# Performance work log

Hardware: AMD Instinct MI355X
Metric: run time of the kernel (lower is better)

The kernel has to match this reference:

```python
import jax, jax.numpy as jnp
import numpy as np
import math

D_MODEL = 512; NHEAD = 8; D_FF = 2048
DS_HEADS = 4; DS_DEPTH = 156; EPS = 1e-5
B = 128; N = 300; M = 300


def _ln(x, g, b):
    m = x.mean(-1, keepdims=True)
    v = ((x - m) ** 2).mean(-1, keepdims=True)
    return (x - m) / jnp.sqrt(v + EPS) * g + b


def _mish(x):
    return x * jnp.tanh(jax.nn.softplus(x))


def _mha(xq, xk, xv, in_w, in_b, out_w, out_b, nhead):
    D = xq.shape[-1]; dh = D // nhead
    wq, wk, wv = jnp.split(in_w, 3, axis=0)
    bq, bk, bv = jnp.split(in_b, 3)
    def proj(x, w, b):
        y = x @ w.T + b
        Bm, Nn, _ = y.shape
        return y.reshape(Bm, Nn, nhead, dh).transpose(0, 2, 1, 3)
    q, k, v = proj(xq, wq, bq), proj(xk, wk, bk), proj(xv, wv, bv)
    s = jnp.einsum('bhqd,bhkd->bhqk', q, k) / math.sqrt(dh)
    p = jax.nn.softmax(s, axis=-1)
    o = jnp.einsum('bhqk,bhkd->bhqd', p, v)
    Bm, _, Nn, _ = o.shape
    o = o.transpose(0, 2, 1, 3).reshape(Bm, Nn, D)
    return o @ out_w.T + out_b


def _custom_weight(p):
    # sequential kinematic-tree averaging on the post-softmax [...,24,24] matrix
    def upd(p, i, j, si, sj):
        return p.at[..., i, j].set((p[..., i, j] + p[..., si, sj]) * 0.5)
    p = upd(p, 0, 6, 0, 3); p = upd(p, 6, 0, 3, 0)
    p = upd(p, 0, 9, 0, 6); p = upd(p, 9, 0, 6, 0)
    for idx in (12, 13, 14):
        p = upd(p, 0, idx, 0, 9); p = upd(p, idx, 0, 9, 0)
    for s, tgt in ((13, 16), (14, 17), (12, 15)):
        p = upd(p, 0, tgt, 0, s); p = upd(p, tgt, 0, s, 0)
    return p


def _ds_attn(x, qk_w, v_w, lw, lb):
    Bm, Nn, _ = x.shape
    comb = jnp.einsum('bnf,fx->bnx', x, qk_w)
    q, k = jnp.split(comb, 2, axis=2)
    v = jnp.einsum('bnf,fx->bnx', x, v_w)
    def heads(y):
        return y.reshape(Bm, Nn, DS_HEADS, DS_DEPTH).transpose(0, 2, 1, 3)
    q, k, v = heads(q), heads(k), heads(v)  # [B,H,N,156]
    qs = q[..., 3:147].reshape(Bm, DS_HEADS, Nn, 24, 6)
    ks = k[..., 3:147].reshape(Bm, DS_HEADS, Nn, 24, 6)
    vs = v[..., 3:147].reshape(Bm, DS_HEADS, Nn, 24, 6)
    s = jnp.einsum('bhnij,bhnkj->bhnik', qs, ks) / math.sqrt(6.0)
    p = _custom_weight(jax.nn.softmax(s, axis=-1))
    o = jnp.einsum('bhnik,bhnkj->bhnij', p, vs).reshape(Bm, DS_HEADS, Nn, 144)
    v = v.at[..., 3:147].set(o)
    v = v.transpose(0, 2, 1, 3).reshape(Bm, Nn, DS_HEADS * DS_DEPTH)
    return v @ lw.T + lb


def _align(x_d, t, w, b):
    tt = t + x_d.mean(axis=-2)           # [B,D]
    h = _mish(tt) @ w.T + b              # [B,2D]
    weight, bias = jnp.split(h, 2, axis=-1)
    return (weight[:, None, :] + 1.0) * x_d + bias[:, None, :]


def _forward(tgt, memory, t, qk_w, v_w, ds_lw, ds_lb,
             ta_in_w, ta_in_b, ta_out_w, ta_out_b,
             ca_in_w, ca_in_b, ca_out_w, ca_out_b,
             l1_w, l1_b, l2_w, l2_b,
             n1_g, n1_b, n2_g, n2_b, n3_g, n3_b, n4_g, n4_b,
             a1_w, a1_b, a2_w, a2_b, a3_w, a3_b):
    x = tgt
    x = x + _ds_attn(_ln(x, n1_g, n1_b), qk_w, v_w, ds_lw, ds_lb)
    xn = _ln(x, n2_g, n2_b)
    x2 = _mha(xn, xn, xn, ta_in_w, ta_in_b, ta_out_w, ta_out_b, NHEAD)
    x = x + _align(x2, t, a1_w, a1_b)
    x3 = _mha(_ln(x, n3_g, n3_b), memory, memory, ca_in_w, ca_in_b, ca_out_w, ca_out_b, NHEAD)
    x = x + _align(x3, t, a2_w, a2_b)
    xn4 = _ln(x, n4_g, n4_b)
    x4 = jax.nn.relu(xn4 @ l1_w.T + l1_b) @ l2_w.T + l2_b
    x = x + _align(x4, t, a3_w, a3_b)
    return x


def setup_inputs():
    key = jax.random.key(0)
    ks = iter(jax.random.split(key, 64))
    def nrm(shape, s=0.02):
        return jax.random.normal(next(ks), shape, dtype=jnp.float32) * s
    z = lambda *shape: jnp.zeros(shape, jnp.float32)
    o = lambda *shape: jnp.ones(shape, jnp.float32)
    D = D_MODEL
    inp = {
        'tgt': jax.random.normal(next(ks), (B, N, D), dtype=jnp.float32),
        'memory': jax.random.normal(next(ks), (B, M, D), dtype=jnp.float32),
        't': jax.random.normal(next(ks), (B, D), dtype=jnp.float32),
        'qk_w': nrm((D, 2 * DS_DEPTH * DS_HEADS)),
        'v_w': nrm((D, DS_DEPTH * DS_HEADS)),
        'ds_lw': nrm((D, DS_DEPTH * DS_HEADS)), 'ds_lb': z(D),
        'ta_in_w': nrm((3 * D, D)), 'ta_in_b': z(3 * D),
        'ta_out_w': nrm((D, D)), 'ta_out_b': z(D),
        'ca_in_w': nrm((3 * D, D)), 'ca_in_b': z(3 * D),
        'ca_out_w': nrm((D, D)), 'ca_out_b': z(D),
        'l1_w': nrm((D_FF, D)), 'l1_b': z(D_FF),
        'l2_w': nrm((D, D_FF)), 'l2_b': z(D),
        'n1_g': o(D), 'n1_b': z(D), 'n2_g': o(D), 'n2_b': z(D),
        'n3_g': o(D), 'n3_b': z(D), 'n4_g': o(D), 'n4_b': z(D),
        'a1_w': nrm((2 * D, D)), 'a1_b': z(2 * D),
        'a2_w': nrm((2 * D, D)), 'a2_b': z(2 * D),
        'a3_w': nrm((2 * D, D)), 'a3_b': z(2 * D),
        'cond_drop_prob': 0,
    }
    return inp


def reference(tgt, memory, t, qk_w, v_w, ds_lw, ds_lb,
              ta_in_w, ta_in_b, ta_out_w, ta_out_b,
              ca_in_w, ca_in_b, ca_out_w, ca_out_b,
              l1_w, l1_b, l2_w, l2_b,
              n1_g, n1_b, n2_g, n2_b, n3_g, n3_b, n4_g, n4_b,
              a1_w, a1_b, a2_w, a2_b, a3_w, a3_b, cond_drop_prob):
    # cond_drop_prob is unused in the torch forward body (dropout eval mode)
    return _forward(tgt, memory, t, qk_w, v_w, ds_lw, ds_lb,
                    ta_in_w, ta_in_b, ta_out_w, ta_out_b,
                    ca_in_w, ca_in_b, ca_out_w, ca_out_b,
                    l1_w, l1_b, l2_w, l2_b,
                    n1_g, n1_b, n2_g, n2_b, n3_g, n3_b, n4_g, n4_b,
                    a1_w, a1_b, a2_w, a2_b, a3_w, a3_b)
```

## Files before the change

kernel.cpp:

```cpp
#include <hip/hip_runtime.h>
#include <math.h>

#define DEV __device__ __forceinline__

static constexpr int BB   = 128;
static constexpr int NN   = 300;
static constexpr int DM   = 512;

typedef __attribute__((ext_vector_type(8))) short short8;
typedef __attribute__((ext_vector_type(4))) float f32x4;

DEV unsigned short f2bf(float f) {
  unsigned u = __float_as_uint(f);
  unsigned r = (u + 0x7fffu + ((u >> 16) & 1u)) >> 16;
  return (unsigned short)r;
}
DEV float bf2f(unsigned short s) { return __uint_as_float((unsigned)s << 16); }
DEV unsigned pack_bf16x2(float a, float b) {
  return (unsigned)f2bf(a) | ((unsigned)f2bf(b) << 16);
}
DEV unsigned pack_trunc(float a, float b) {
  return (__float_as_uint(a) >> 16) | (__float_as_uint(b) & 0xffff0000u);
}

DEV void gld16(const void* g, void* l) {
  __builtin_amdgcn_global_load_lds(
      (const __attribute__((address_space(1))) unsigned int*)g,
      (__attribute__((address_space(3))) unsigned int*)l,
      16, 0, 0);
}

__global__ __launch_bounds__(256) void ln_kernel(
    const float* __restrict__ X, const float* __restrict__ g,
    const float* __restrict__ b, unsigned short* __restrict__ Y, int rows)
{
  int wv = threadIdx.x >> 6, lane = threadIdx.x & 63;
  int row = blockIdx.x * 4 + wv;
  if (row >= rows) return;
  const float* xp = X + (size_t)row * DM;
  float v[8]; float s = 0.f, s2 = 0.f;
#pragma unroll
  for (int j = 0; j < 8; j++) {
    v[j] = xp[lane + 64 * j]; s += v[j]; s2 += v[j] * v[j];
  }
#pragma unroll
  for (int o = 32; o >= 1; o >>= 1) { s += __shfl_xor(s, o); s2 += __shfl_xor(s2, o); }
  float mean = s * (1.f / 512.f);
  float var  = s2 * (1.f / 512.f) - mean * mean;
  float rstd = rsqrtf(var + 1e-5f);
  unsigned short* yp = Y + (size_t)row * DM;
#pragma unroll
  for (int j = 0; j < 8; j++) {
    int c = lane + 64 * j;
    yp[c] = f2bf((v[j] - mean) * rstd * g[c] + b[c]);
  }
}

__global__ __launch_bounds__(256) void cvt_bf16(
    const float* __restrict__ in, unsigned short* __restrict__ out, int n4)
{
  int i = blockIdx.x * 256 + threadIdx.x;
  if (i >= n4) return;
  float4 v = ((const float4*)in)[i];
  union { unsigned short s[4]; uint2 u; } o;
  o.s[0] = f2bf(v.x); o.s[1] = f2bf(v.y); o.s[2] = f2bf(v.z); o.s[3] = f2bf(v.w);
  *(uint2*)&out[(size_t)i * 4] = o.u;
}

__global__ __launch_bounds__(256) void cvt_pad_bf16(
    const float* __restrict__ in, unsigned short* __restrict__ out,
    int R, int C, int Cpad)
{
  int idx = blockIdx.x * 256 + threadIdx.x;
  int r = idx / Cpad, c = idx % Cpad;
  if (r >= R) return;
  out[idx] = (c < C) ? f2bf(in[(size_t)r * C + c]) : (unsigned short)0;
}

__global__ __launch_bounds__(256) void transpose_bf16(
    const float* __restrict__ in, unsigned short* __restrict__ out,
    int R, int Ccols, int Cpad)
{
  __shared__ float t[32][33];
  int c0 = blockIdx.x * 32, r0 = blockIdx.y * 32;
  int x = threadIdx.x & 31, y = threadIdx.x >> 5;
#pragma unroll
  for (int dy = 0; dy < 32; dy += 8) {
    int r = r0 + y + dy, c = c0 + x;
    t[y + dy][x] = (r < R && c < Ccols) ? in[(size_t)r * Ccols + c] : 0.f;
  }
  __syncthreads();
#pragma unroll
  for (int dy = 0; dy < 32; dy += 8) {
    int c = c0 + y + dy, r = r0 + x;
    if (c < Cpad && r < R) out[(size_t)c * R + r] = f2bf(t[x][y + dy]);
  }
}

template<int EPI>
__global__ __launch_bounds__(256) void gemm_bb(
    const unsigned short* __restrict__ A, int lda,
    const unsigned short* __restrict__ W, int ldw,
    const float* __restrict__ bias,
    const float* __restrict__ R, int ldr,
    void* __restrict__ Cv, int ldc,
    int M, int K, int NC)
{
  __shared__ __align__(16) unsigned short As[128 * 32];
  __shared__ __align__(16) unsigned short Bs[128 * 32];
  const int tid = threadIdx.x;
  const int wave = tid >> 6, lane = tid & 63;
  const int wr = wave >> 1, wc = wave & 1;
  const int quad = lane >> 4, l16 = lane & 15;

  const unsigned nx = gridDim.x, nwg = nx * gridDim.y;
  const unsigned orig = blockIdx.y * nx + blockIdx.x;
  const unsigned qq = nwg >> 3, rr = nwg & 7;
  const unsigned xcd = orig & 7, idx = orig >> 3;
  const unsigned swz = (xcd < rr) ? (xcd * (qq + 1) + idx)
                                  : (rr * (qq + 1) + (xcd - rr) * qq + idx);
  const int n0 = (int)(swz % nx) * 128;
  const int m0 = (int)(swz / nx) * 128;

  int ra = m0 + (tid >> 2);
  int ra0 = (ra      >= M) ? M - 1 : ra;
  int ra1 = (ra + 64 >= M) ? M - 1 : ra + 64;
  const unsigned short* a0 = A + (size_t)ra0 * lda + (tid & 3) * 8;
  const unsigned short* a1 = A + (size_t)ra1 * lda + (tid & 3) * 8;
  const unsigned short* b0 = W + (size_t)(n0 + (tid >> 2)) * ldw + (tid & 3) * 8;
  const unsigned short* b1 = b0 + (size_t)64 * ldw;
  unsigned short* dA0 = &As[wave * 512];
  unsigned short* dA1 = &As[2048 + wave * 512];
  unsigned short* dB0 = &Bs[wave * 512];
  unsigned short* dB1 = &Bs[2048 + wave * 512];

  f32x4 acc[4][4];
#pragma unroll
  for (int i = 0; i < 4; i++)
#pragma unroll
    for (int j = 0; j < 4; j++) acc[i][j] = (f32x4){0.f, 0.f, 0.f, 0.f};

  for (int k0 = 0; k0 < K; k0 += 32) {
    gld16(a0 + k0, dA0);
    gld16(a1 + k0, dA1);
    gld16(b0 + k0, dB0);
    gld16(b1 + k0, dB1);
    __syncthreads();
    short8 af[4], bq[4];
#pragma unroll
    for (int i = 0; i < 4; i++)
      af[i] = *(const short8*)&As[(wr * 64 + i * 16 + l16) * 32 + quad * 8];
#pragma unroll
    for (int j = 0; j < 4; j++)
      bq[j] = *(const short8*)&Bs[(wc * 64 + j * 16 + l16) * 32 + quad * 8];
#pragma unroll
    for (int i = 0; i < 4; i++)
#pragma unroll
      for (int j = 0; j < 4; j++)
        acc[i][j] = __builtin_amdgcn_mfma_f32_16x16x32_bf16(af[i], bq[j], acc[i][j], 0, 0, 0);
    __syncthreads();
  }

#pragma unroll
  for (int i = 0; i < 4; i++) {
    int rbase = m0 + wr * 64 + i * 16 + quad * 4;
#pragma unroll
    for (int r = 0; r < 4; r++) {
      int row = rbase + r;
      if (row < M) {
        size_t rowc = (size_t)row * ldc;
#pragma unroll
        for (int j = 0; j < 4; j++) {
          int col = n0 + wc * 64 + j * 16 + l16;
          if (col < NC) {
            float e = acc[i][j][r];
            if (EPI == 1 || EPI == 2 || EPI == 3 || EPI == 5) e += bias[col];
            if (EPI == 3) e += R[(size_t)row * ldr + col];
            if (EPI == 2) {
              ((unsigned short*)Cv)[rowc + col] = f2bf(fmaxf(e, 0.f));
            } else if (EPI == 5 || EPI == 6) {
              ((unsigned short*)Cv)[rowc + col] = f2bf(e);
            } else {
              ((float*)Cv)[rowc + col] = e;
            }
          }
        }
      }
    }
  }
}

__global__ __launch_bounds__(256) void ds_attn_kernel(
    const float* __restrict__ COMB, unsigned short* __restrict__ V)
{
  __shared__ float ks[4][2][24][6];
  __shared__ float vs[4][2][24][6];
  int wv = threadIdx.x >> 6, lane = threadIdx.x & 63;
  int half = lane >> 5, i = lane & 31;
  int u  = blockIdx.x * 4 + wv;
  int bn = u >> 1, hp = u & 1;
  int h  = hp * 2 + half;
  size_t cbase = (size_t)bn * 1248 + h * 156 + 3;
  size_t vbase = (size_t)bn * 640  + h * 156 + 3;

  float q[6];
  if (i < 24) {
#pragma unroll
    for (int j = 0; j < 6; j++) {
      q[j]                 = COMB[cbase + i * 6 + j];
      ks[wv][half][i][j]   = COMB[cbase + 624 + i * 6 + j];
      vs[wv][half][i][j]   = bf2f(V[vbase + i * 6 + j]);
    }
  } else {
#pragma unroll
    for (int j = 0; j < 6; j++) q[j] = 0.f;
  }
  __syncthreads();

  float p[24];
#pragma unroll
  for (int k = 0; k < 24; k++) p[k] = 0.f;

  if (i < 24) {
    float mx = -1e30f;
#pragma unroll
    for (int k = 0; k < 24; k++) {
      float s = 0.f;
#pragma unroll
      for (int j = 0; j < 6; j++) s += q[j] * ks[wv][half][k][j];
      s *= 0.4082482904638631f;
      p[k] = s; mx = fmaxf(mx, s);
    }
    float sum = 0.f;
#pragma unroll
    for (int k = 0; k < 24; k++) { p[k] = __expf(p[k] - mx); sum += p[k]; }
    float inv = 1.f / sum;
#pragma unroll
    for (int k = 0; k < 24; k++) p[k] *= inv;
  }

  {
    float c = p[0];
    float t;
    t = __shfl(c, 3, 32);  if (i == 6) c = (c + t) * 0.5f;
    t = __shfl(c, 6, 32);  if (i == 9) c = (c + t) * 0.5f;
    t = __shfl(c, 9, 32);  if (i >= 12 && i <= 14) c = (c + t) * 0.5f;
    int src = (i >= 3) ? (i - 3) : 0;
    t = __shfl(c, src, 32); if (i >= 15 && i <= 17) c = (c + t) * 0.5f;
    p[0] = c;
  }
  if (i == 0) {
    p[6]  = (p[6]  + p[3])  * 0.5f;
    p[9]  = (p[9]  + p[6])  * 0.5f;
    p[12] = (p[12] + p[9])  * 0.5f;
    p[13] = (p[13] + p[9])  * 0.5f;
    p[14] = (p[14] + p[9])  * 0.5f;
    p[16] = (p[16] + p[13]) * 0.5f;
    p[17] = (p[17] + p[14]) * 0.5f;
    p[15] = (p[15] + p[12]) * 0.5f;
  }

  if (i < 24) {
    float o[6] = {0.f, 0.f, 0.f, 0.f, 0.f, 0.f};
#pragma unroll
    for (int k = 0; k < 24; k++) {
#pragma unroll
      for (int j = 0; j < 6; j++) o[j] += p[k] * vs[wv][half][k][j];
    }
#pragma unroll
    for (int j = 0; j < 6; j++) V[vbase + i * 6 + j] = f2bf(o[j]);
  }
}

__global__ __launch_bounds__(512) void mha_mfma(
    const unsigned short* __restrict__ Qp, int ldq, int qoff,
    const unsigned short* __restrict__ KVp, int ldkv, int koff, int voff,
    unsigned short* __restrict__ Op, float scale)
{
  __shared__ __align__(16) unsigned short Ksh[304 * 72];
  __shared__ __align__(16) unsigned short Vt[64 * 328];
  __shared__ __align__(16) unsigned short Pt[8][16 * 40];
  const int bh = blockIdx.x, b = bh >> 3, h = bh & 7;
  const int tid = threadIdx.x, wv = tid >> 6, lane = tid & 63;
  const int quad = lane >> 4, l16 = lane & 15;
  const size_t kbase = (size_t)b * NN * ldkv + koff + h * 64;
  const size_t vbase = (size_t)b * NN * ldkv + voff + h * 64;

  for (int f = tid; f < 304 * 8; f += 512) {
    int rk = f >> 3, c8 = (f & 7) * 8;
    short8 w;
    if (rk < 300) {
      w = *(const short8*)(KVp + kbase + (size_t)rk * ldkv + c8);
    } else {
      union { uint4 u; short8 s; } z; z.u = make_uint4(0u, 0u, 0u, 0u); w = z.s;
    }
    *(short8*)&Ksh[rk * 72 + c8] = w;
  }
  for (int f = tid; f < 64 * 164; f += 512) {
    int d = f & 63, s0 = (f >> 6) * 2;
    unsigned w = 0u;
    if (s0 < 300) {
      unsigned short v0 = KVp[vbase + (size_t)s0 * ldkv + d];
      unsigned short v1 = (s0 + 1 < 300) ? KVp[vbase + (size_t)(s0 + 1) * ldkv + d]
                                         : (unsigned short)0;
      w = (unsigned)v0 | ((unsigned)v1 << 16);
    }
    *(unsigned*)&Vt[d * 328 + s0] = w;
  }
  __syncthreads();

  unsigned short* pt = &Pt[wv][0];

  for (int qt = wv; qt < 19; qt += 8) {
    int qrow = qt * 16 + l16; if (qrow > 299) qrow = 299;
    const unsigned short* qp = Qp + (size_t)(b * NN + qrow) * ldq + qoff + h * 64 + quad * 8;
    short8 qf[2];
    qf[0] = *(const short8*)(qp);
    qf[1] = *(const short8*)(qp + 32);

    f32x4 sacc[19];
#pragma unroll
    for (int t = 0; t < 19; t++) {
      short8 k0 = *(const short8*)&Ksh[(t * 16 + l16) * 72 + quad * 8];
      short8 k1 = *(const short8*)&Ksh[(t * 16 + l16) * 72 + 32 + quad * 8];
      f32x4 a = (f32x4){0.f, 0.f, 0.f, 0.f};
      a = __builtin_amdgcn_mfma_f32_16x16x32_bf16(k0, qf[0], a, 0, 0, 0);
      a = __builtin_amdgcn_mfma_f32_16x16x32_bf16(k1, qf[1], a, 0, 0, 0);
      sacc[t] = a;
    }

    float mx = -1e30f;
#pragma unroll
    for (int t = 0; t < 19; t++)
#pragma unroll
      for (int r = 0; r < 4; r++) mx = fmaxf(mx, sacc[t][r]);
    mx = fmaxf(mx, __shfl_xor(mx, 16));
    mx = fmaxf(mx, __shfl_xor(mx, 32));
    float sum = 0.f;
#pragma unroll
    for (int t = 0; t < 19; t++) {
#pragma unroll
      for (int r = 0; r < 4; r++) {
        float p = __expf((sacc[t][r] - mx) * scale);
        if (t == 18 && quad == 3) p = 0.f;
        sacc[t][r] = p; sum += p;
      }
    }
    sum += __shfl_xor(sum, 16);
    sum += __shfl_xor(sum, 32);
    float inv = 1.f / sum;

    f32x4 oacc[4];
#pragma unroll
    for (int dt = 0; dt < 4; dt++) oacc[dt] = (f32x4){0.f, 0.f, 0.f, 0.f};
#pragma unroll
    for (int c = 0; c < 10; c++) {
#pragma unroll
      for (int tic = 0; tic < 2; tic++) {
        int t = 2 * c + tic;
        unsigned w0 = 0u, w1 = 0u;
        if (t < 19) {
          w0 = pack_trunc(sacc[t][0], sacc[t][1]);
          w1 = pack_trunc(sacc[t][2], sacc[t][3]);
        }
        *(unsigned*)&pt[l16 * 40 + tic * 16 + quad * 4]     = w0;
        *(unsigned*)&pt[l16 * 40 + tic * 16 + quad * 4 + 2] = w1;
      }
      short8 pa = *(const short8*)&pt[l16 * 40 + quad * 8];
#pragma unroll
      for (int dt = 0; dt < 4; dt++) {
        short8 vb = *(const short8*)&Vt[(dt * 16 + l16) * 328 + c * 32 + quad * 8];
        oacc[dt] = __builtin_amdgcn_mfma_f32_16x16x32_bf16(pa, vb, oacc[dt], 0, 0, 0);
      }
    }

#pragma unroll
    for (int r = 0; r < 4; r++) {
      int row = qt * 16 + quad * 4 + r;
      float iv = __shfl(inv, quad * 4 + r);
      if (row < 300) {
        unsigned short* op = Op + (size_t)(b * NN + row) * DM + h * 64 + l16;
#pragma unroll
        for (int dt = 0; dt < 4; dt++)
          op[dt * 16] = f2bf(oacc[dt][r] * iv);
      }
    }
  }
}

__global__ __launch_bounds__(256) void colmean_mish(
    const float* __restrict__ Y, const float* __restrict__ tvec,
    unsigned short* __restrict__ mm)
{
  int g = blockIdx.x * 256 + threadIdx.x;
  int b = g >> 9, d = g & 511;
  const float* yp = Y + (size_t)b * NN * DM + d;
  float s = 0.f;
  for (int n = 0; n < NN; n++) s += yp[(size_t)n * DM];
  float v = tvec[g] + s * (1.f / 300.f);
  float sp = (v > 20.f) ? v : log1pf(__expf(v));
  mm[g] = f2bf(v * tanhf(sp));
}

__global__ __launch_bounds__(256) void align_apply(
    float* __restrict__ X, const float* __restrict__ Y,
    const float* __restrict__ H)
{
  int idx = blockIdx.x * 256 + threadIdx.x;
  int row = idx >> 7;
  int d4  = (idx & 127) * 4;
  int b   = row / NN;
  float4 y = *(const float4*)&Y[(size_t)row * DM + d4];
  float4 x = *(const float4*)&X[(size_t)row * DM + d4];
  const float* hw = H + (size_t)b * 1024 + d4;
  const float* hb = hw + 512;
  x.x += (hw[0] + 1.f) * y.x + hb[0];
  x.y += (hw[1] + 1.f) * y.y + hb[1];
  x.z += (hw[2] + 1.f) * y.z + hb[2];
  x.w += (hw[3] + 1.f) * y.w + hb[3];
  *(float4*)&X[(size_t)row * DM + d4] = x;
}

extern "C" void kernel_launch(void* const* d_in, const int* in_sizes, int n_in,
                              void* d_out, int out_size, void* d_ws, size_t ws_size,
                              hipStream_t stream)
{
  const float* tgt      = (const float*)d_in[0];
  const float* memory   = (const float*)d_in[1];
  const float* tvec     = (const float*)d_in[2];
  const float* qk_w     = (const float*)d_in[3];
  const float* v_w      = (const float*)d_in[4];
  const float* ds_lw    = (const float*)d_in[5];
  const float* ds_lb    = (const float*)d_in[6];
  const float* ta_in_w  = (const float*)d_in[7];
  const float* ta_in_b  = (const float*)d_in[8];
  const float* ta_out_w = (const float*)d_in[9];
  const float* ta_out_b = (const float*)d_in[10];
  const float* ca_in_w  = (const float*)d_in[11];
  const float* ca_in_b  = (const float*)d_in[12];
  const float* ca_out_w = (const float*)d_in[13];
  const float* ca_out_b = (const float*)d_in[14];
  const float* l1_w     = (const float*)d_in[15];
  const float* l1_b     = (const float*)d_in[16];
  const float* l2_w     = (const float*)d_in[17];
  const float* l2_b     = (const float*)d_in[18];
  const float* n1_g = (const float*)d_in[19]; const float* n1_b = (const float*)d_in[20];
  const float* n2_g = (const float*)d_in[21]; const float* n2_b = (const float*)d_in[22];
  const float* n3_g = (const float*)d_in[23]; const float* n3_b = (const float*)d_in[24];
  const float* n4_g = (const float*)d_in[25]; const float* n4_b = (const float*)d_in[26];
  const float* a1_w = (const float*)d_in[27]; const float* a1_b = (const float*)d_in[28];
  const float* a2_w = (const float*)d_in[29]; const float* a2_b = (const float*)d_in[30];
  const float* a3_w = (const float*)d_in[31]; const float* a3_b = (const float*)d_in[32];

  const size_t W_QKT = 1280ULL * 512 * 2;
  const size_t W_VT  = 640ULL  * 512 * 2;
  const size_t W_TAI = 1536ULL * 512 * 2;
  const size_t W_TAO = 512ULL  * 512 * 2;
  const size_t W_CAI = 1536ULL * 512 * 2;
  const size_t W_CAO = 512ULL  * 512 * 2;
  const size_t W_L1  = 2048ULL * 512 * 2;
  const size_t W_L2  = 512ULL  * 2048 * 2;
  const size_t W_DSL = 512ULL  * 640 * 2;
  const size_t W_AX  = 1024ULL * 512 * 2;
  const size_t W_MEM = (size_t)BB * NN * 512 * 2;
  const size_t fixedB = W_QKT + W_VT + W_TAI + W_TAO + W_CAI + W_CAO
                      + W_L1 + W_L2 + W_DSL + 3 * W_AX + W_MEM;
  const size_t per_b = 300ULL * (1024 + 4992 + 1280 + 2048) + 1024 + 4096;
  int Bc = 128;
  while (Bc > 16 && fixedB + (size_t)Bc * per_b > ws_size) Bc >>= 1;
  const int rows = Bc * NN;
  const int mB   = (rows + 127) / 128;
  const int aB   = (Bc + 127) / 128;
  const int nchunks = BB / Bc;

  char* p = (char*)d_ws;
  unsigned short* qkTh  = (unsigned short*)p; p += W_QKT;
  unsigned short* vTh   = (unsigned short*)p; p += W_VT;
  unsigned short* taiWh = (unsigned short*)p; p += W_TAI;
  unsigned short* taoWh = (unsigned short*)p; p += W_TAO;
  unsigned short* caiWh = (unsigned short*)p; p += W_CAI;
  unsigned short* caoWh = (unsigned short*)p; p += W_CAO;
  unsigned short* l1Wh  = (unsigned short*)p; p += W_L1;
  unsigned short* l2Wh  = (unsigned short*)p; p += W_L2;
  unsigned short* dslWh = (unsigned short*)p; p += W_DSL;
  unsigned short* a1Wh  = (unsigned short*)p; p += W_AX;
  unsigned short* a2Wh  = (unsigned short*)p; p += W_AX;
  unsigned short* a3Wh  = (unsigned short*)p; p += W_AX;
  unsigned short* memh  = (unsigned short*)p; p += W_MEM;
  unsigned short* XNh   = (unsigned short*)p; p += (size_t)rows * 512 * 2;
  char* SCRB = p;                             p += (size_t)rows * 4992;
  unsigned short* Vdsh  = (unsigned short*)p; p += (size_t)rows * 640 * 2;
  float* Yb  = (float*)p; p += (size_t)rows * 512 * 4;
  unsigned short* MMh = (unsigned short*)p;   p += (size_t)Bc * 512 * 2;
  float* Hb  = (float*)p;

  float* COMB = (float*)SCRB;
  unsigned short* QKVh = (unsigned short*)SCRB;
  unsigned short* T2h  = (unsigned short*)SCRB;

  dim3 thr(256);

  transpose_bf16<<<dim3(40, 16), thr, 0, stream>>>(qk_w, qkTh, 512, 1248, 1280);
  transpose_bf16<<<dim3(20, 16), thr, 0, stream>>>(v_w,  vTh,  512, 624, 640);
  cvt_pad_bf16<<<dim3(512 * 640 / 256), thr, 0, stream>>>(ds_lw, dslWh, 512, 624, 640);
  auto cvt = [&](const float* src, unsigned short* dst, size_t n) {
    int n4 = (int)(n / 4);
    cvt_bf16<<<dim3((n4 + 255) / 256), thr, 0, stream>>>(src, dst, n4);
  };
  cvt(ta_in_w,  taiWh, 1536ULL * 512);
  cvt(ta_out_w, taoWh, 512ULL * 512);
  cvt(ca_in_w,  caiWh, 1536ULL * 512);
  cvt(ca_out_w, caoWh, 512ULL * 512);
  cvt(l1_w,     l1Wh,  2048ULL * 512);
  cvt(l2_w,     l2Wh,  512ULL * 2048);
  cvt(a1_w,     a1Wh,  1024ULL * 512);
  cvt(a2_w,     a2Wh,  1024ULL * 512);
  cvt(a3_w,     a3Wh,  1024ULL * 512);
  cvt(memory,   memh,  (size_t)BB * NN * 512);

  for (int c = 0; c < nchunks; ++c) {
    const size_t roff = (size_t)c * Bc * NN * DM;
    const float* tgtC = tgt    + roff;
    const float* tC   = tvec   + (size_t)c * Bc * 512;
    const unsigned short* memhC = memh + roff;
    float*       XC   = (float*)d_out + roff;

    ln_kernel<<<rows / 4, thr, 0, stream>>>(tgtC, n1_g, n1_b, XNh, rows);
    gemm_bb<0><<<dim3(10, mB), thr, 0, stream>>>(XNh, 512, qkTh, 512, nullptr, nullptr, 0, COMB, 1248, rows, 512, 1248);
    gemm_bb<6><<<dim3(5, mB),  thr, 0, stream>>>(XNh, 512, vTh,  512, nullptr, nullptr, 0, Vdsh, 640,  rows, 512, 640);
    ds_attn_kernel<<<rows / 2, thr, 0, stream>>>(COMB, Vdsh);
    gemm_bb<3><<<dim3(4, mB),  thr, 0, stream>>>(Vdsh, 640, dslWh, 640, ds_lb, tgtC, 512, XC, 512, rows, 640, 512);

    ln_kernel<<<rows / 4, thr, 0, stream>>>(XC, n2_g, n2_b, XNh, rows);
    gemm_bb<5><<<dim3(12, mB), thr, 0, stream>>>(XNh, 512, taiWh, 512, ta_in_b, nullptr, 0, QKVh, 1536, rows, 512, 1536);
    mha_mfma<<<Bc * 8, 512, 0, stream>>>(QKVh, 1536, 0, QKVh, 1536, 512, 1024, XNh, 0.125f);
    gemm_bb<1><<<dim3(4, mB),  thr, 0, stream>>>(XNh, 512, taoWh, 512, ta_out_b, nullptr, 0, Yb, 512, rows, 512, 512);
    colmean_mish<<<Bc * 2, thr, 0, stream>>>(Yb, tC, MMh);
    gemm_bb<1><<<dim3(8, aB),  thr, 0, stream>>>(MMh, 512, a1Wh, 512, a1_b, nullptr, 0, Hb, 1024, Bc, 512, 1024);
    align_apply<<<rows / 2, thr, 0, stream>>>(XC, Yb, Hb);

    ln_kernel<<<rows / 4, thr, 0, stream>>>(XC, n3_g, n3_b, XNh, rows);
    gemm_bb<5><<<dim3(4, mB),  thr, 0, stream>>>(XNh, 512, caiWh, 512, ca_in_b, nullptr, 0, QKVh, 1536, rows, 512, 512);
    gemm_bb<5><<<dim3(8, mB),  thr, 0, stream>>>(memhC, 512, caiWh + 512 * 512, 512, ca_in_b + 512, nullptr, 0, QKVh + 512, 1536, rows, 512, 1024);
    mha_mfma<<<Bc * 8, 512, 0, stream>>>(QKVh, 1536, 0, QKVh, 1536, 512, 1024, XNh, 0.125f);
    gemm_bb<1><<<dim3(4, mB),  thr, 0, stream>>>(XNh, 512, caoWh, 512, ca_out_b, nullptr, 0, Yb, 512, rows, 512, 512);
    colmean_mish<<<Bc * 2, thr, 0, stream>>>(Yb, tC, MMh);
    gemm_bb<1><<<dim3(8, aB),  thr, 0, stream>>>(MMh, 512, a2Wh, 512, a2_b, nullptr, 0, Hb, 1024, Bc, 512, 1024);
    align_apply<<<rows / 2, thr, 0, stream>>>(XC, Yb, Hb);

    ln_kernel<<<rows / 4, thr, 0, stream>>>(XC, n4_g, n4_b, XNh, rows);
    gemm_bb<2><<<dim3(16, mB), thr, 0, stream>>>(XNh, 512, l1Wh, 512, l1_b, nullptr, 0, T2h, 2048, rows, 512, 2048);
    gemm_bb<1><<<dim3(4, mB),  thr, 0, stream>>>(T2h, 2048, l2Wh, 2048, l2_b, nullptr, 0, Yb, 512, rows, 2048, 512);
    colmean_mish<<<Bc * 2, thr, 0, stream>>>(Yb, tC, MMh);
    gemm_bb<1><<<dim3(8, aB),  thr, 0, stream>>>(MMh, 512, a3Wh, 512, a3_b, nullptr, 0, Hb, 1024, Bc, 512, 1024);
    align_apply<<<rows / 2, thr, 0, stream>>>(XC, Yb, Hb);
  }
}
```

Measured before the change: 2.321 ms.

## Fuse align-apply with following layernorm; stage Q and output through LDS in MHA

Two align_apply+ln_kernel pairs are replaced by a single align_ln kernel that applies the FiLM-style update, writes X back, and produces the normalized bf16 output in one pass, saving a read of X and a launch. In the attention kernel, Q is now loaded cooperatively into shared memory alongside K, and outputs are staged through the per-wave LDS scratch so each row is written with 16-byte vector stores instead of scattered 2-byte stores. This adds roughly 44 KB more LDS per block, which may cut occupancy.

```diff
diff --git a/kernel.cpp b/kernel.cpp
--- a/kernel.cpp
+++ b/kernel.cpp
@@ -53,6 +53,41 @@
   for (int j = 0; j < 8; j++) {
     int c = lane + 64 * j;
     yp[c] = f2bf((v[j] - mean) * rstd * g[c] + b[c]);
+  }
+}
+
+__global__ __launch_bounds__(256) void align_ln(
+    float* __restrict__ X, const float* __restrict__ Y,
+    const float* __restrict__ H,
+    const float* __restrict__ g, const float* __restrict__ bb,
+    unsigned short* __restrict__ XN)
+{
+  int wv = threadIdx.x >> 6, lane = threadIdx.x & 63;
+  int row = blockIdx.x * 4 + wv;
+  int b = row / NN;
+  float* xp = X + (size_t)row * DM;
+  const float* yp = Y + (size_t)row * DM;
+  const float* hw = H + (size_t)b * 1024;
+  const float* hb = hw + 512;
+  float v[8]; float s = 0.f, s2 = 0.f;
+#pragma unroll
+  for (int j = 0; j < 8; j++) {
+    int c = lane + 64 * j;
+    float xv = xp[c] + (hw[c] + 1.f) * yp[c] + hb[c];
+    v[j] = xv; s += xv; s2 += xv * xv;
+  }
+#pragma unroll
+  for (int j = 0; j < 8; j++) xp[lane + 64 * j] = v[j];
+#pragma unroll
+  for (int o = 32; o >= 1; o >>= 1) { s += __shfl_xor(s, o); s2 += __shfl_xor(s2, o); }
+  float mean = s * (1.f / 512.f);
+  float var  = s2 * (1.f / 512.f) - mean * mean;
+  float rstd = rsqrtf(var + 1e-5f);
+  unsigned short* yn = XN + (size_t)row * DM;
+#pragma unroll
+  for (int j = 0; j < 8; j++) {
+    int c = lane + 64 * j;
+    yn[c] = f2bf((v[j] - mean) * rstd * g[c] + bb[c]);
   }
 }
 
@@ -278,23 +313,28 @@
     unsigned short* __restrict__ Op, float scale)
 {
   __shared__ __align__(16) unsigned short Ksh[304 * 72];
+  __shared__ __align__(16) unsigned short Qsh[304 * 72];
   __shared__ __align__(16) unsigned short Vt[64 * 328];
-  __shared__ __align__(16) unsigned short Pt[8][16 * 40];
+  __shared__ __align__(16) unsigned short Pt[8][16 * 68];
   const int bh = blockIdx.x, b = bh >> 3, h = bh & 7;
   const int tid = threadIdx.x, wv = tid >> 6, lane = tid & 63;
   const int quad = lane >> 4, l16 = lane & 15;
   const size_t kbase = (size_t)b * NN * ldkv + koff + h * 64;
   const size_t vbase = (size_t)b * NN * ldkv + voff + h * 64;
+  const size_t qbase = (size_t)b * NN * ldq  + qoff + h * 64;
 
   for (int f = tid; f < 304 * 8; f += 512) {
     int rk = f >> 3, c8 = (f & 7) * 8;
-    short8 w;
+    short8 wk, wq;
     if (rk < 300) {
-      w = *(const short8*)(KVp + kbase + (size_t)rk * ldkv + c8);
+      wk = *(const short8*)(KVp + kbase + (size_t)rk * ldkv + c8);
+      wq = *(const short8*)(Qp  + qbase + (size_t)rk * ldq  + c8);
     } else {
-      union { uint4 u; short8 s; } z; z.u = make_uint4(0u, 0u, 0u, 0u); w = z.s;
-    }
-    *(short8*)&Ksh[rk * 72 + c8] = w;
+      union { uint4 u; short8 s; } z; z.u = make_uint4(0u, 0u, 0u, 0u);
+      wk = z.s; wq = z.s;
+    }
+    *(short8*)&Ksh[rk * 72 + c8] = wk;
+    *(short8*)&Qsh[rk * 72 + c8] = wq;
   }
   for (int f = tid; f < 64 * 164; f += 512) {
     int d = f & 63, s0 = (f >> 6) * 2;
@@ -312,11 +352,10 @@
   unsigned short* pt = &Pt[wv][0];
 
   for (int qt = wv; qt < 19; qt += 8) {
-    int qrow = qt * 16 + l16; if (qrow > 299) qrow = 299;
-    const unsigned short* qp = Qp + (size_t)(b * NN + qrow) * ldq + qoff + h * 64 + quad * 8;
+    int qr = qt * 16 + l16;
     short8 qf[2];
-    qf[0] = *(const short8*)(qp);
-    qf[1] = *(const short8*)(qp + 32);
+    qf[0] = *(const short8*)&Qsh[qr * 72 + quad * 8];
+    qf[1] = *(const short8*)&Qsh[qr * 72 + 32 + quad * 8];
 
     f32x4 sacc[19];
 #pragma unroll
@@ -363,10 +402,10 @@
           w0 = pack_trunc(sacc[t][0], sacc[t][1]);
           w1 = pack_trunc(sacc[t][2], sacc[t][3]);
         }
-        *(unsigned*)&pt[l16 * 40 + tic * 16 + quad * 4]     = w0;
-        *(unsigned*)&pt[l16 * 40 + tic * 16 + quad * 4 + 2] = w1;
+        *(unsigned*)&pt[l16 * 68 + tic * 16 + quad * 4]     = w0;
+        *(unsigned*)&pt[l16 * 68 + tic * 16 + quad * 4 + 2] = w1;
       }
-      short8 pa = *(const short8*)&pt[l16 * 40 + quad * 8];
+      short8 pa = *(const short8*)&pt[l16 * 68 + quad * 8];
 #pragma unroll
       for (int dt = 0; dt < 4; dt++) {
         short8 vb = *(const short8*)&Vt[(dt * 16 + l16) * 328 + c * 32 + quad * 8];
@@ -376,14 +415,19 @@
 
 #pragma unroll
     for (int r = 0; r < 4; r++) {
-      int row = qt * 16 + quad * 4 + r;
       float iv = __shfl(inv, quad * 4 + r);
-      if (row < 300) {
-        unsigned short* op = Op + (size_t)(b * NN + row) * DM + h * 64 + l16;
-#pragma unroll
-        for (int dt = 0; dt < 4; dt++)
-          op[dt * 16] = f2bf(oacc[dt][r] * iv);
-      }
+#pragma unroll
+      for (int dt = 0; dt < 4; dt++)
+        pt[(quad * 4 + r) * 68 + dt * 16 + l16] = f2bf(oacc[dt][r] * iv);
+    }
+#pragma unroll
+    for (int rep = 0; rep < 2; rep++) {
+      int idx = rep * 64 + lane;
+      int rl = idx >> 3, seg = idx & 7;
+      int row = qt * 16 + rl;
+      uint4 w = *(const uint4*)&pt[rl * 68 + seg * 8];
+      if (row < 300)
+        *(uint4*)(Op + (size_t)(b * NN + row) * DM + h * 64 + seg * 8) = w;
     }
   }
 }
@@ -537,18 +581,16 @@
     gemm_bb<1><<<dim3(4, mB),  thr, 0, stream>>>(XNh, 512, taoWh, 512, ta_out_b, nullptr, 0, Yb, 512, rows, 512, 512);
     colmean_mish<<<Bc * 2, thr, 0, stream>>>(Yb, tC, MMh);
     gemm_bb<1><<<dim3(8, aB),  thr, 0, stream>>>(MMh, 512, a1Wh, 512, a1_b, nullptr, 0, Hb, 1024, Bc, 512, 1024);
-    align_apply<<<rows / 2, thr, 0, stream>>>(XC, Yb, Hb);
-
-    ln_kernel<<<rows / 4, thr, 0, stream>>>(XC, n3_g, n3_b, XNh, rows);
+    align_ln<<<rows / 4, thr, 0, stream>>>(XC, Yb, Hb, n3_g, n3_b, XNh);
+
     gemm_bb<5><<<dim3(4, mB),  thr, 0, stream>>>(XNh, 512, caiWh, 512, ca_in_b, nullptr, 0, QKVh, 1536, rows, 512, 512);
     gemm_bb<5><<<dim3(8, mB),  thr, 0, stream>>>(memhC, 512, caiWh + 512 * 512, 512, ca_in_b + 512, nullptr, 0, QKVh + 512, 1536, rows, 512, 1024);
     mha_mfma<<<Bc * 8, 512, 0, stream>>>(QKVh, 1536, 0, QKVh, 1536, 512, 1024, XNh, 0.125f);
     gemm_bb<1><<<dim3(4, mB),  thr, 0, stream>>>(XNh, 512, caoWh, 512, ca_out_b, nullptr, 0, Yb, 512, rows, 512, 512);
     colmean_mish<<<Bc * 2, thr, 0, stream>>>(Yb, tC, MMh);
     gemm_bb<1><<<dim3(8, aB),  thr, 0, stream>>>(MMh, 512, a2Wh, 512, a2_b, nullptr, 0, Hb, 1024, Bc, 512, 1024);
-    align_apply<<<rows / 2, thr, 0, stream>>>(XC, Yb, Hb);
-
-    ln_kernel<<<rows / 4, thr, 0, stream>>>(XC, n4_g, n4_b, XNh, rows);
+    align_ln<<<rows / 4, thr, 0, stream>>>(XC, Yb, Hb, n4_g, n4_b, XNh);
+
     gemm_bb<2><<<dim3(16, mB), thr, 0, stream>>>(XNh, 512, l1Wh, 512, l1_b, nullptr, 0, T2h, 2048, rows, 512, 2048);
     gemm_bb<1><<<dim3(4, mB),  thr, 0, stream>>>(T2h, 2048, l2Wh, 2048, l2_b, nullptr, 0, Yb, 512, rows, 2048, 512);
     colmean_mish<<<Bc * 2, thr, 0, stream>>>(Yb, tC, MMh);
```

New measurement: 2.295 ms. Within noise of the previous version (-1.1%).
